# Performance work log

Measured on AMD Instinct MI355X. Metric: run time of the kernel, lower is better.

## Reference

```python
import jax, jax.numpy as jnp
import numpy as np

H = 768
NH = 12
HD = H // NH
FF = 3072
EPS = 1e-12
SCALE = 1.0 / (HD ** 0.5)


def _ln(x, g, b):
    m = jnp.mean(x, axis=-1, keepdims=True)
    v = jnp.mean((x - m) ** 2, axis=-1, keepdims=True)
    return (x - m) * jax.lax.rsqrt(v + EPS) * g + b


def setup_inputs() -> dict:
    key = jax.random.key(0)
    ks = jax.random.split(key, 16)
    B, Q, S, T = 8, 64, 48, 128
    s = 0.02
    return {
        "q": jax.random.normal(ks[0], (B, Q, H), jnp.float32),
        "k": jax.random.normal(ks[1], (B, S, T, H), jnp.float32),
        "mask": jax.random.randint(ks[2], (B, S, T), 0, 2, jnp.int32),
        "Wq": jax.random.normal(ks[3], (H, H), jnp.float32) * s,
        "Wkv": jax.random.normal(ks[4], (H, H), jnp.float32) * s,
        "Wo": jax.random.normal(ks[5], (H, H), jnp.float32) * s,
        "bo": jnp.zeros((H,), jnp.float32),
        "ln1_g": jnp.ones((H,), jnp.float32),
        "ln1_b": jnp.zeros((H,), jnp.float32),
        "W1": jax.random.normal(ks[6], (H, FF), jnp.float32) * s,
        "b1": jnp.zeros((FF,), jnp.float32),
        "W2": jax.random.normal(ks[7], (FF, H), jnp.float32) * s,
        "b2": jnp.zeros((H,), jnp.float32),
        "ln2_g": jnp.ones((H,), jnp.float32),
        "ln2_b": jnp.zeros((H,), jnp.float32),
    }


def reference(q, k, mask, Wq, Wkv, Wo, bo, ln1_g, ln1_b, W1, b1, W2, b2, ln2_g, ln2_b):
    B, Q, _ = q.shape
    _, S, T, _ = k.shape
    # projections (no bias)
    qp = (q @ Wq).reshape(B, Q, NH, HD)            # [b,q,h,d]
    kv = (k @ Wkv).reshape(B, S, T, NH, HD)        # [b,s,t,h,d]
    # broadcast-query grouped attention: softmax only over token dim t
    scores = jnp.einsum('bqhd,bsthd->bhqst', qp, kv) * SCALE
    scores = scores + mask.astype(scores.dtype)[:, None, None, :, :] * -10000.0
    alpha = jax.nn.softmax(scores, axis=-1)        # dropout is identity in eval
    res = jnp.einsum('bhqst,bsthd->bqshd', alpha, kv).reshape(B, Q, S, H)
    # BertSelfOutput with zero residual (residual=False)
    attn_out = _ln(res @ Wo + bo, ln1_g, ln1_b)    # [b,q,s,H]
    # FFN
    ffn = jax.nn.gelu(attn_out @ W1 + b1, approximate=False) @ W2 + b2
    return _ln(attn_out + ffn, ln2_g, ln2_b)
```

## Files before the change

### kernel.cpp

```cpp
#include <hip/hip_runtime.h>
#include <hip/hip_bf16.h>
#include <math.h>

#define B_ 8
#define Q_ 64
#define S_ 48
#define T_ 128
#define H_ 768
#define NH_ 12
#define HD_ 64
#define FF_ 3072

typedef float f32x4 __attribute__((ext_vector_type(4)));
typedef short s16x8 __attribute__((ext_vector_type(8)));
typedef short s16x4 __attribute__((ext_vector_type(4)));

__device__ __forceinline__ float ldT(const float* p, size_t i) { return p[i]; }
__device__ __forceinline__ float ldT(const __hip_bfloat16* p, size_t i) { return __bfloat162float(p[i]); }
__device__ __forceinline__ void stT(float* p, size_t i, float v) { p[i] = v; }
__device__ __forceinline__ void stT(__hip_bfloat16* p, size_t i, float v) { p[i] = __float2bfloat16(v); }

__device__ __forceinline__ short f2bf(float f) {
  __hip_bfloat16 h = __float2bfloat16(f);
  return *reinterpret_cast<short*>(&h);
}

__device__ __forceinline__ float gelu_f(float x) {
  return 0.5f * x * (1.0f + erff(x * 0.70710678118654752f));
}

__device__ __forceinline__ void gld_lds16(const void* g, void* l) {
  __builtin_amdgcn_global_load_lds(
      (const __attribute__((address_space(1))) void*)g,
      (__attribute__((address_space(3))) void*)l, 16, 0, 0);
}

#define FENCE() asm volatile("" ::: "memory")
#define BARRIER() do { FENCE(); __builtin_amdgcn_s_barrier(); FENCE(); } while (0)
#define WAITV(n) asm volatile("s_waitcnt vmcnt(" #n ")" ::: "memory")

template<int K, typename OT, bool BIAS, bool GELU>
__global__ __launch_bounds__(512, 2) void gemm8p(
    const __hip_bfloat16* __restrict__ A,
    const __hip_bfloat16* __restrict__ BT,
    const float* __restrict__ bias, OT* __restrict__ C,
    int N, int nbx)
{
  constexpr int NT = K / 64;
  static_assert(NT % 3 == 0, "K/64 must be divisible by 3");
  __shared__ __align__(16) char sm[3 * 49152];

  int wg = blockIdx.x;
  const int q8 = gridDim.x >> 3;
  wg = (wg & 7) * q8 + (wg >> 3);
  const int bm = wg / nbx;
  const int bn = wg % nbx;
  const int m0 = bm * 128, n0 = bn * 256;

  const int tid = threadIdx.x;
  const int lane = tid & 63;
  const int wid = tid >> 6;
  const int wr = wid >> 2;
  const int wc = wid & 3;
  const int kcg = lane >> 4;
  const int rl = lane & 15;

  const __hip_bfloat16* gA[2];
  const __hip_bfloat16* gB[4];
  #pragma unroll
  for (int r = 0; r < 2; ++r) {
    const int c = tid + r * 512, row = c >> 3, slot = c & 7;
    const int kc = slot ^ (row & 7);
    gA[r] = A + (size_t)(m0 + row) * K + kc * 8;
  }
  #pragma unroll
  for (int r = 0; r < 4; ++r) {
    const int c = tid + r * 512, row = c >> 3, slot = c & 7;
    const int kc = slot ^ (row & 7);
    gB[r] = BT + (size_t)(n0 + row) * K + kc * 8;
  }

  auto stageA = [&](char* bb) {
    gld_lds16(gA[0], bb + tid * 16);
    gld_lds16(gA[1], bb + (tid + 512) * 16);
    gA[0] += 64; gA[1] += 64;
  };
  auto stageB1 = [&](char* bb) {
    gld_lds16(gB[0], bb + 16384 + tid * 16);
    gld_lds16(gB[1], bb + 16384 + (tid + 512) * 16);
    gB[0] += 64; gB[1] += 64;
  };
  auto stageB2 = [&](char* bb) {
    gld_lds16(gB[2], bb + 16384 + (tid + 1024) * 16);
    gld_lds16(gB[3], bb + 16384 + (tid + 1536) * 16);
    gB[2] += 64; gB[3] += 64;
  };

  int offA[4][2], offB[4][2];
  #pragma unroll
  for (int mf = 0; mf < 4; ++mf)
    #pragma unroll
    for (int kch = 0; kch < 2; ++kch) {
      const int row = wr * 64 + mf * 16 + rl;
      const int ch = kch * 4 + kcg;
      offA[mf][kch] = row * 128 + ((ch ^ (row & 7)) << 4);
    }
  #pragma unroll
  for (int nf = 0; nf < 4; ++nf)
    #pragma unroll
    for (int kch = 0; kch < 2; ++kch) {
      const int row = wc * 64 + nf * 16 + rl;
      const int ch = kch * 4 + kcg;
      offB[nf][kch] = 16384 + row * 128 + ((ch ^ (row & 7)) << 4);
    }

  f32x4 acc[4][4] = {};

  stageA(sm); stageB1(sm); stageB2(sm);
  stageA(sm + 49152); stageB1(sm + 49152); stageB2(sm + 49152);
  WAITV(6);
  BARRIER();

  auto tile_body = [&](char* cb, char* nb, bool doStage, bool last) {
    s16x8 af[4][2], bf[4][2];
    #pragma unroll
    for (int mf = 0; mf < 2; ++mf)
      #pragma unroll
      for (int kch = 0; kch < 2; ++kch)
        af[mf][kch] = *(const s16x8*)(cb + offA[mf][kch]);
    #pragma unroll
    for (int nf = 0; nf < 2; ++nf)
      #pragma unroll
      for (int kch = 0; kch < 2; ++kch)
        bf[nf][kch] = *(const s16x8*)(cb + offB[nf][kch]);
    if (doStage) stageA(nb);
    BARRIER();
    __builtin_amdgcn_s_setprio(1);
    #pragma unroll
    for (int kch = 0; kch < 2; ++kch)
      #pragma unroll
      for (int mf = 0; mf < 2; ++mf)
        #pragma unroll
        for (int nf = 0; nf < 2; ++nf)
          acc[mf][nf] = __builtin_amdgcn_mfma_f32_16x16x32_bf16(
              af[mf][kch], bf[nf][kch], acc[mf][nf], 0, 0, 0);
    __builtin_amdgcn_s_setprio(0);
    BARRIER();
    #pragma unroll
    for (int nf = 2; nf < 4; ++nf)
      #pragma unroll
      for (int kch = 0; kch < 2; ++kch)
        bf[nf][kch] = *(const s16x8*)(cb + offB[nf][kch]);
    if (doStage) stageB1(nb);
    BARRIER();
    __builtin_amdgcn_s_setprio(1);
    #pragma unroll
    for (int kch = 0; kch < 2; ++kch)
      #pragma unroll
      for (int mf = 0; mf < 2; ++mf)
        #pragma unroll
        for (int nf = 2; nf < 4; ++nf)
          acc[mf][nf] = __builtin_amdgcn_mfma_f32_16x16x32_bf16(
              af[mf][kch], bf[nf][kch], acc[mf][nf], 0, 0, 0);
    __builtin_amdgcn_s_setprio(0);
    BARRIER();
    #pragma unroll
    for (int mf = 2; mf < 4; ++mf)
      #pragma unroll
      for (int kch = 0; kch < 2; ++kch)
        af[mf][kch] = *(const s16x8*)(cb + offA[mf][kch]);
    if (doStage) stageB2(nb);
    BARRIER();
    __builtin_amdgcn_s_setprio(1);
    #pragma unroll
    for (int kch = 0; kch < 2; ++kch)
      #pragma unroll
      for (int mf = 2; mf < 4; ++mf)
        #pragma unroll
        for (int nf = 0; nf < 2; ++nf)
          acc[mf][nf] = __builtin_amdgcn_mfma_f32_16x16x32_bf16(
              af[mf][kch], bf[nf][kch], acc[mf][nf], 0, 0, 0);
    __builtin_amdgcn_s_setprio(0);
    BARRIER();
    __builtin_amdgcn_s_setprio(1);
    #pragma unroll
    for (int kch = 0; kch < 2; ++kch)
      #pragma unroll
      for (int mf = 2; mf < 4; ++mf)
        #pragma unroll
        for (int nf = 2; nf < 4; ++nf)
          acc[mf][nf] = __builtin_amdgcn_mfma_f32_16x16x32_bf16(
              af[mf][kch], bf[nf][kch], acc[mf][nf], 0, 0, 0);
    __builtin_amdgcn_s_setprio(0);
    if (!last) {
      if (doStage) WAITV(6);
      else         WAITV(0);
      BARRIER();
    }
  };

  char* b0 = sm;
  char* b1 = sm + 49152;
  char* b2 = sm + 2 * 49152;
  #pragma unroll 1
  for (int t = 0; t < NT; t += 3) {
    tile_body(b0, b2, t + 2 < NT, t + 1 == NT);
    tile_body(b1, b0, t + 3 < NT, t + 2 == NT);
    tile_body(b2, b1, t + 4 < NT, t + 3 == NT);
  }

  const int colb = n0 + wc * 64 + rl;
  const int rowb = m0 + wr * 64 + (lane >> 4) * 4;
  float bv[4];
  #pragma unroll
  for (int nf = 0; nf < 4; ++nf) bv[nf] = BIAS ? bias[colb + nf * 16] : 0.0f;
  #pragma unroll
  for (int mf = 0; mf < 4; ++mf) {
    #pragma unroll
    for (int r = 0; r < 4; ++r) {
      const int row = rowb + mf * 16 + r;
      #pragma unroll
      for (int nf = 0; nf < 4; ++nf) {
        float v = acc[mf][nf][r] + bv[nf];
        if (GELU) v = gelu_f(v);
        stT(C, (size_t)row * N + colb + nf * 16, v);
      }
    }
  }
}

template<typename OT>
__global__ __launch_bounds__(256) void gemm64(
    const float* __restrict__ A, const float* __restrict__ W,
    OT* __restrict__ C, int M, int N, int K)
{
  __shared__ float As[16][65];
  __shared__ float Ws[16][65];
  const int tid = threadIdx.x;
  const int m0 = blockIdx.y * 64;
  const int n0 = blockIdx.x * 64;
  const int tx = (tid & 15) * 4;
  const int ty = (tid >> 4) * 4;
  float acc[4][4] = {};

  for (int k0 = 0; k0 < K; k0 += 16) {
    #pragma unroll
    for (int r = 0; r < 4; ++r) {
      int idx = tid + r * 256;
      int mm = idx >> 4, kk = idx & 15;
      As[kk][mm] = A[(size_t)(m0 + mm) * K + (k0 + kk)];
    }
    #pragma unroll
    for (int r = 0; r < 4; ++r) {
      int idx = tid + r * 256;
      int kk = idx >> 6, nn = idx & 63;
      Ws[kk][nn] = W[(size_t)(k0 + kk) * N + (n0 + nn)];
    }
    __syncthreads();
    #pragma unroll
    for (int kk = 0; kk < 16; ++kk) {
      float a[4], b[4];
      #pragma unroll
      for (int i = 0; i < 4; ++i) a[i] = As[kk][ty + i];
      #pragma unroll
      for (int j = 0; j < 4; ++j) b[j] = Ws[kk][tx + j];
      #pragma unroll
      for (int i = 0; i < 4; ++i)
        #pragma unroll
        for (int j = 0; j < 4; ++j) acc[i][j] += a[i] * b[j];
    }
    __syncthreads();
  }
  #pragma unroll
  for (int i = 0; i < 4; ++i)
    #pragma unroll
    for (int j = 0; j < 4; ++j)
      stT(C, (size_t)(m0 + ty + i) * N + (n0 + tx + j), acc[i][j]);
}

__global__ __launch_bounds__(256) void transpose_cast(
    const float* __restrict__ W, __hip_bfloat16* __restrict__ WT, int K, int N)
{
  __shared__ float t[32][33];
  const int n0 = blockIdx.x * 32, k0 = blockIdx.y * 32;
  const int x = threadIdx.x & 31, y4 = (threadIdx.x >> 5) * 4;
  #pragma unroll
  for (int i = 0; i < 4; ++i)
    t[y4 + i][x] = W[(size_t)(k0 + y4 + i) * N + n0 + x];
  __syncthreads();
  #pragma unroll
  for (int i = 0; i < 4; ++i)
    WT[(size_t)(n0 + y4 + i) * K + k0 + x] = __float2bfloat16(t[x][y4 + i]);
}

__global__ __launch_bounds__(256) void cast_f32_bf16(
    const float* __restrict__ x, __hip_bfloat16* __restrict__ y, size_t n4)
{
  const size_t i = (size_t)blockIdx.x * 256 + threadIdx.x;
  if (i >= n4) return;
  const float4 v = ((const float4*)x)[i];
  __hip_bfloat16 o[4] = { __float2bfloat16(v.x), __float2bfloat16(v.y),
                          __float2bfloat16(v.z), __float2bfloat16(v.w) };
  *(ushort4*)(y + i * 4) = *(ushort4*)o;
}

__global__ __launch_bounds__(256) void attn_mfma(
    const __hip_bfloat16* __restrict__ qp,
    const __hip_bfloat16* __restrict__ kvp,
    const int* __restrict__ mask,
    __hip_bfloat16* __restrict__ res)
{
  const int s = blockIdx.x, h = blockIdx.y, b = blockIdx.z;
  __shared__ __align__(16) char lds[66048];
  char* Ks = lds;
  char* VT = lds + 16384;
  char* SC = lds + 32768;
  float* mv = (float*)(lds + 65536);

  const int tid = threadIdx.x;
  const int lane = tid & 63;
  const int wid = tid >> 6;
  const int wr = wid >> 1, wc = wid & 1;
  const int kcg = lane >> 4, rl = lane & 15;

  if (tid < 128) mv[tid] = (float)mask[((size_t)b * S_ + s) * T_ + tid] * -10000.0f;

  {
    const __hip_bfloat16* qb = qp + ((size_t)b * Q_) * H_ + h * HD_;
    #pragma unroll
    for (int r = 0; r < 2; ++r) {
      const int c = tid + r * 256;
      const int qq = c >> 3, sc = c & 7;
      const int kc8 = sc ^ (qq & 7);
      gld_lds16(qb + (size_t)qq * H_ + kc8 * 8, SC + c * 16);
    }
  }
  {
    const int kc8 = tid & 7, tg = tid >> 3;
    const int t0 = tg * 4;
    const __hip_bfloat16* kb = kvp + (((size_t)b * S_ + s) * T_) * H_ + h * HD_ + kc8 * 8;
    s16x8 r0 = *(const s16x8*)(kb + (size_t)(t0 + 0) * H_);
    s16x8 r1 = *(const s16x8*)(kb + (size_t)(t0 + 1) * H_);
    s16x8 r2 = *(const s16x8*)(kb + (size_t)(t0 + 2) * H_);
    s16x8 r3 = *(const s16x8*)(kb + (size_t)(t0 + 3) * H_);
    *(s16x8*)(Ks + (t0 + 0) * 128 + ((kc8 ^ ((t0 + 0) & 7)) << 4)) = r0;
    *(s16x8*)(Ks + (t0 + 1) * 128 + ((kc8 ^ ((t0 + 1) & 7)) << 4)) = r1;
    *(s16x8*)(Ks + (t0 + 2) * 128 + ((kc8 ^ ((t0 + 2) & 7)) << 4)) = r2;
    *(s16x8*)(Ks + (t0 + 3) * 128 + ((kc8 ^ ((t0 + 3) & 7)) << 4)) = r3;
    const int tc = tg >> 1;
    const int toff = (tg & 1) * 8;
    #pragma unroll
    for (int j = 0; j < 8; ++j) {
      s16x4 v4 = { r0[j], r1[j], r2[j], r3[j] };
      const int d = kc8 * 8 + j;
      *(s16x4*)(VT + d * 256 + ((tc ^ (d & 15)) << 4) + toff) = v4;
    }
  }
  __syncthreads();

  f32x4 acc[2][4] = {};
  {
    s16x8 af[2][2], bf[2][4];
    #pragma unroll
    for (int kk = 0; kk < 2; ++kk) {
      #pragma unroll
      for (int m = 0; m < 2; ++m) {
        const int q = wr * 32 + m * 16 + rl;
        const int kc8 = kk * 4 + kcg;
        af[kk][m] = *(const s16x8*)(SC + q * 128 + ((kc8 ^ (q & 7)) << 4));
      }
      #pragma unroll
      for (int n = 0; n < 4; ++n) {
        const int t = wc * 64 + n * 16 + rl;
        const int kc8 = kk * 4 + kcg;
        bf[kk][n] = *(const s16x8*)(Ks + t * 128 + ((kc8 ^ (t & 7)) << 4));
      }
    }
    #pragma unroll
    for (int kk = 0; kk < 2; ++kk)
      #pragma unroll
      for (int m = 0; m < 2; ++m)
        #pragma unroll
        for (int n = 0; n < 4; ++n)
          acc[m][n] = __builtin_amdgcn_mfma_f32_16x16x32_bf16(af[kk][m], bf[kk][n], acc[m][n], 0, 0, 0);
  }
  __syncthreads();

  #pragma unroll
  for (int m = 0; m < 2; ++m)
    #pragma unroll
    for (int n = 0; n < 4; ++n)
      #pragma unroll
      for (int r = 0; r < 4; ++r) {
        const int q = wr * 32 + m * 16 + (lane >> 4) * 4 + r;
        const int t = wc * 64 + n * 16 + rl;
        const int tc32 = t >> 2;
        *(float*)(SC + q * 512 + ((tc32 ^ (q & 31)) << 4) + (t & 3) * 4) =
            acc[m][n][r] * 0.125f + mv[t];
      }
  __syncthreads();

  {
    const int q = tid >> 2, quarter = tid & 3;
    float vals[32];
    #pragma unroll
    for (int j = 0; j < 8; ++j) {
      const int tc32 = quarter * 8 + j;
      const f32x4 c = *(const f32x4*)(SC + q * 512 + ((tc32 ^ (q & 31)) << 4));
      vals[j * 4 + 0] = c[0]; vals[j * 4 + 1] = c[1];
      vals[j * 4 + 2] = c[2]; vals[j * 4 + 3] = c[3];
    }
    float mx = -1e30f;
    #pragma unroll
    for (int i = 0; i < 32; ++i) mx = fmaxf(mx, vals[i]);
    mx = fmaxf(mx, __shfl_xor(mx, 1, 64));
    mx = fmaxf(mx, __shfl_xor(mx, 2, 64));
    float sum = 0.0f;
    #pragma unroll
    for (int i = 0; i < 32; ++i) { vals[i] = expf(vals[i] - mx); sum += vals[i]; }
    sum += __shfl_xor(sum, 1, 64);
    sum += __shfl_xor(sum, 2, 64);
    const float inv = 1.0f / sum;
    #pragma unroll
    for (int jj = 0; jj < 4; ++jj) {
      const int tcp = quarter * 4 + jj;
      s16x8 pk;
      #pragma unroll
      for (int i = 0; i < 8; ++i) pk[i] = f2bf(vals[jj * 8 + i] * inv);
      *(s16x8*)(SC + q * 512 + ((tcp ^ (q & 15)) << 4)) = pk;
    }
  }
  __syncthreads();

  f32x4 oacc[2][2] = {};
  #pragma unroll
  for (int kt = 0; kt < 4; ++kt) {
    s16x8 pa[2], vb[2];
    #pragma unroll
    for (int m = 0; m < 2; ++m) {
      const int q = wr * 32 + m * 16 + rl;
      const int tcp = kt * 4 + kcg;
      pa[m] = *(const s16x8*)(SC + q * 512 + ((tcp ^ (q & 15)) << 4));
    }
    #pragma unroll
    for (int n = 0; n < 2; ++n) {
      const int d = wc * 32 + n * 16 + rl;
      const int tc = kt * 4 + kcg;
      vb[n] = *(const s16x8*)(VT + d * 256 + ((tc ^ (d & 15)) << 4));
    }
    #pragma unroll
    for (int m = 0; m < 2; ++m)
      #pragma unroll
      for (int n = 0; n < 2; ++n)
        oacc[m][n] = __builtin_amdgcn_mfma_f32_16x16x32_bf16(pa[m], vb[n], oacc[m][n], 0, 0, 0);
  }
  #pragma unroll
  for (int m = 0; m < 2; ++m)
    #pragma unroll
    for (int n = 0; n < 2; ++n)
      #pragma unroll
      for (int r = 0; r < 4; ++r) {
        const int q = wr * 32 + m * 16 + (lane >> 4) * 4 + r;
        const int d = wc * 32 + n * 16 + rl;
        res[(((size_t)b * Q_ + q) * S_ + s) * H_ + h * HD_ + d] =
            __float2bfloat16(oacc[m][n][r]);
      }
}

template<bool ADD, typename IT, typename OT>
__global__ __launch_bounds__(256) void ln_kernel(
    const IT* __restrict__ X, const IT* __restrict__ X2,
    const float* __restrict__ g, const float* __restrict__ bta,
    OT* __restrict__ Y)
{
  const size_t row = blockIdx.x;
  const int tid = threadIdx.x;
  float v[3];
  #pragma unroll
  for (int i = 0; i < 3; ++i) {
    int c = tid + i * 256;
    v[i] = ldT(X, row * H_ + c);
    if (ADD) v[i] += ldT(X2, row * H_ + c);
  }
  float sum = v[0] + v[1] + v[2];
  #pragma unroll
  for (int off = 32; off > 0; off >>= 1) sum += __shfl_down(sum, off, 64);
  __shared__ float red[8];
  const int w = tid >> 6;
  if ((tid & 63) == 0) red[w] = sum;
  __syncthreads();
  const float mean = (red[0] + red[1] + red[2] + red[3]) * (1.0f / 768.0f);
  float vs = 0.0f;
  #pragma unroll
  for (int i = 0; i < 3; ++i) { v[i] -= mean; vs += v[i] * v[i]; }
  #pragma unroll
  for (int off = 32; off > 0; off >>= 1) vs += __shfl_down(vs, off, 64);
  if ((tid & 63) == 0) red[4 + w] = vs;
  __syncthreads();
  const float rstd = rsqrtf((red[4] + red[5] + red[6] + red[7]) * (1.0f / 768.0f) + 1e-12f);
  #pragma unroll
  for (int i = 0; i < 3; ++i) {
    int c = tid + i * 256;
    stT(Y, row * H_ + c, v[i] * rstd * g[c] + bta[c]);
  }
}

extern "C" void kernel_launch(void* const* d_in, const int* in_sizes, int n_in,
                              void* d_out, int out_size, void* d_ws, size_t ws_size,
                              hipStream_t stream) {
  const float* q    = (const float*)d_in[0];
  const float* k    = (const float*)d_in[1];
  const int*   mask = (const int*)d_in[2];
  const float* Wq   = (const float*)d_in[3];
  const float* Wkv  = (const float*)d_in[4];
  const float* Wo   = (const float*)d_in[5];
  const float* bo   = (const float*)d_in[6];
  const float* ln1g = (const float*)d_in[7];
  const float* ln1b = (const float*)d_in[8];
  const float* W1   = (const float*)d_in[9];
  const float* b1   = (const float*)d_in[10];
  const float* W2   = (const float*)d_in[11];
  const float* b2   = (const float*)d_in[12];
  const float* ln2g = (const float*)d_in[13];
  const float* ln2b = (const float*)d_in[14];
  float* out = (float*)d_out;

  const int MROWS = B_ * Q_ * S_;
  const int KVROWS = B_ * S_ * T_;

  char* ws = (char*)d_ws;
  __hip_bfloat16* kbf  = (__hip_bfloat16*)ws;
  __hip_bfloat16* kvp  = (__hip_bfloat16*)(ws + 75497472);
  __hip_bfloat16* ffn1 = (__hip_bfloat16*)ws;
  __hip_bfloat16* ares = (__hip_bfloat16*)(ws + 150994944);
  __hip_bfloat16* ffn2 = ares;
  __hip_bfloat16* aln  = (__hip_bfloat16*)(ws + 188743680);
  __hip_bfloat16* qp   = (__hip_bfloat16*)(ws + 226492416);
  __hip_bfloat16* WkvT = (__hip_bfloat16*)(ws + 228065280);
  __hip_bfloat16* WoT  = (__hip_bfloat16*)(ws + 229244928);
  __hip_bfloat16* W1T  = (__hip_bfloat16*)(ws + 230424576);
  __hip_bfloat16* W2T  = (__hip_bfloat16*)(ws + 235143168);

  dim3 blk(256);
  dim3 blk8(512);

  transpose_cast<<<dim3(24, 24), blk, 0, stream>>>(Wkv, WkvT, H_, H_);
  transpose_cast<<<dim3(24, 24), blk, 0, stream>>>(Wo, WoT, H_, H_);
  transpose_cast<<<dim3(96, 24), blk, 0, stream>>>(W1, W1T, H_, FF_);
  transpose_cast<<<dim3(24, 96), blk, 0, stream>>>(W2, W2T, FF_, H_);
  cast_f32_bf16<<<dim3((KVROWS * H_ / 4 + 255) / 256), blk, 0, stream>>>(
      k, kbf, (size_t)KVROWS * H_ / 4);

  gemm64<__hip_bfloat16><<<dim3(H_ / 64, 512 / 64), blk, 0, stream>>>(
      q, Wq, qp, 512, H_, H_);
  gemm8p<768, __hip_bfloat16, false, false>
      <<<dim3((KVROWS / 128) * (H_ / 256)), blk8, 0, stream>>>(
      kbf, WkvT, nullptr, kvp, H_, H_ / 256);
  attn_mfma<<<dim3(S_, NH_, B_), blk, 0, stream>>>(qp, kvp, mask, ares);
  gemm8p<768, float, true, false>
      <<<dim3((MROWS / 128) * (H_ / 256)), blk8, 0, stream>>>(
      ares, WoT, bo, out, H_, H_ / 256);
  ln_kernel<false, float, __hip_bfloat16><<<MROWS, blk, 0, stream>>>(
      out, nullptr, ln1g, ln1b, aln);
  gemm8p<768, __hip_bfloat16, true, true>
      <<<dim3((MROWS / 128) * (FF_ / 256)), blk8, 0, stream>>>(
      aln, W1T, b1, ffn1, FF_, FF_ / 256);
  gemm8p<3072, __hip_bfloat16, true, false>
      <<<dim3((MROWS / 128) * (H_ / 256)), blk8, 0, stream>>>(
      ffn1, W2T, b2, ffn2, H_, H_ / 256);
  ln_kernel<true, __hip_bfloat16, float><<<MROWS, blk, 0, stream>>>(
      aln, ffn2, ln2g, ln2b, out);
}
```

Baseline: 679.7 us.

## Enlarge GEMM tiles to 256x256 with a nine-slot LDS ring pipeline

```diff
diff --git a/kernel.cpp b/kernel.cpp
--- a/kernel.cpp
+++ b/kernel.cpp
@@ -40,182 +40,162 @@
 #define WAITV(n) asm volatile("s_waitcnt vmcnt(" #n ")" ::: "memory")
 
 template<int K, typename OT, bool BIAS, bool GELU>
-__global__ __launch_bounds__(512, 2) void gemm8p(
+__global__ __launch_bounds__(512, 2) void gemm9r(
     const __hip_bfloat16* __restrict__ A,
     const __hip_bfloat16* __restrict__ BT,
     const float* __restrict__ bias, OT* __restrict__ C,
     int N, int nbx)
 {
   constexpr int NT = K / 64;
-  static_assert(NT % 3 == 0, "K/64 must be divisible by 3");
-  __shared__ __align__(16) char sm[3 * 49152];
+  static_assert(NT >= 3, "need at least 3 K-tiles");
+  __shared__ __align__(16) char sm[9 * 16384];
 
   int wg = blockIdx.x;
   const int q8 = gridDim.x >> 3;
   wg = (wg & 7) * q8 + (wg >> 3);
   const int bm = wg / nbx;
   const int bn = wg % nbx;
-  const int m0 = bm * 128, n0 = bn * 256;
+  const int m0 = bm * 256, n0 = bn * 256;
 
   const int tid = threadIdx.x;
   const int lane = tid & 63;
   const int wid = tid >> 6;
-  const int wr = wid >> 2;
+  const int wm = wid >> 2;
   const int wc = wid & 3;
+  const int bh = wc >> 1;
   const int kcg = lane >> 4;
   const int rl = lane & 15;
 
-  const __hip_bfloat16* gA[2];
-  const __hip_bfloat16* gB[4];
-  #pragma unroll
-  for (int r = 0; r < 2; ++r) {
-    const int c = tid + r * 512, row = c >> 3, slot = c & 7;
-    const int kc = slot ^ (row & 7);
-    gA[r] = A + (size_t)(m0 + row) * K + kc * 8;
-  }
-  #pragma unroll
-  for (int r = 0; r < 4; ++r) {
-    const int c = tid + r * 512, row = c >> 3, slot = c & 7;
-    const int kc = slot ^ (row & 7);
-    gB[r] = BT + (size_t)(n0 + row) * K + kc * 8;
-  }
-
-  auto stageA = [&](char* bb) {
-    gld_lds16(gA[0], bb + tid * 16);
-    gld_lds16(gA[1], bb + (tid + 512) * 16);
-    gA[0] += 64; gA[1] += 64;
+  const int c1r = tid >> 3;
+  const int c1k = (tid & 7) ^ (c1r & 7);
+
+  auto stage_slot = [&](int slot) {
+    const int tile = slot >> 2, half = slot & 3;
+    const __hip_bfloat16* mb =
+        (half < 2 ? A + (size_t)m0 * K : BT + (size_t)n0 * K)
+        + (size_t)(half & 1) * 128 * K + tile * 64;
+    char* lb = sm + (slot % 9) * 16384;
+    gld_lds16(mb + (size_t)c1r * K + c1k * 8, lb + tid * 16);
+    gld_lds16(mb + (size_t)(c1r + 64) * K + c1k * 8, lb + (tid + 512) * 16);
   };
-  auto stageB1 = [&](char* bb) {
-    gld_lds16(gB[0], bb + 16384 + tid * 16);
-    gld_lds16(gB[1], bb + 16384 + (tid + 512) * 16);
-    gB[0] += 64; gB[1] += 64;
-  };
-  auto stageB2 = [&](char* bb) {
-    gld_lds16(gB[2], bb + 16384 + (tid + 1024) * 16);
-    gld_lds16(gB[3], bb + 16384 + (tid + 1536) * 16);
-    gB[2] += 64; gB[3] += 64;
-  };
-
-  int offA[4][2], offB[4][2];
-  #pragma unroll
-  for (int mf = 0; mf < 4; ++mf)
-    #pragma unroll
-    for (int kch = 0; kch < 2; ++kch) {
-      const int row = wr * 64 + mf * 16 + rl;
-      const int ch = kch * 4 + kcg;
-      offA[mf][kch] = row * 128 + ((ch ^ (row & 7)) << 4);
-    }
-  #pragma unroll
-  for (int nf = 0; nf < 4; ++nf)
-    #pragma unroll
-    for (int kch = 0; kch < 2; ++kch) {
-      const int row = wc * 64 + nf * 16 + rl;
-      const int ch = kch * 4 + kcg;
-      offB[nf][kch] = 16384 + row * 128 + ((ch ^ (row & 7)) << 4);
-    }
-
-  f32x4 acc[4][4] = {};
-
-  stageA(sm); stageB1(sm); stageB2(sm);
-  stageA(sm + 49152); stageB1(sm + 49152); stageB2(sm + 49152);
-  WAITV(6);
+
+  int woffA[8], woffB[4];
+  #pragma unroll
+  for (int mf = 0; mf < 8; ++mf) {
+    const int lr = mf * 16 + rl;
+    woffA[mf] = lr * 128 + ((kcg ^ (lr & 7)) << 4);
+  }
+  #pragma unroll
+  for (int nf = 0; nf < 4; ++nf) {
+    const int lr = (wc & 1) * 64 + nf * 16 + rl;
+    woffB[nf] = lr * 128 + ((kcg ^ (lr & 7)) << 4);
+  }
+
+  f32x4 acc[8][4] = {};
+
+  stage_slot(0); stage_slot(1); stage_slot(2); stage_slot(3); stage_slot(4);
+  WAITV(2);
   BARRIER();
 
-  auto tile_body = [&](char* cb, char* nb, bool doStage, bool last) {
-    s16x8 af[4][2], bf[4][2];
-    #pragma unroll
-    for (int mf = 0; mf < 2; ++mf)
+  int ringT = 0;
+  #pragma unroll 1
+  for (int t = 0; t < NT; ++t) {
+    int rA = ringT + wm;      if (rA >= 9) rA -= 9;
+    int rB = ringT + 2 + bh;  if (rB >= 9) rB -= 9;
+    const char* baseA = sm + rA * 16384;
+    const char* baseB = sm + rB * 16384;
+
+    s16x8 af0[4][2], af1[4][2], bf[2][2];
+
+    #pragma unroll
+    for (int mf = 0; mf < 4; ++mf)
       #pragma unroll
       for (int kch = 0; kch < 2; ++kch)
-        af[mf][kch] = *(const s16x8*)(cb + offA[mf][kch]);
+        af0[mf][kch] = *(const s16x8*)(baseA + (woffA[mf] ^ (kch << 6)));
     #pragma unroll
     for (int nf = 0; nf < 2; ++nf)
       #pragma unroll
       for (int kch = 0; kch < 2; ++kch)
-        bf[nf][kch] = *(const s16x8*)(cb + offB[nf][kch]);
-    if (doStage) stageA(nb);
+        bf[nf][kch] = *(const s16x8*)(baseB + (woffB[nf] ^ (kch << 6)));
+    if (4 * t + 5 < 4 * NT) stage_slot(4 * t + 5);
     BARRIER();
     __builtin_amdgcn_s_setprio(1);
     #pragma unroll
     for (int kch = 0; kch < 2; ++kch)
       #pragma unroll
-      for (int mf = 0; mf < 2; ++mf)
+      for (int mf = 0; mf < 4; ++mf)
         #pragma unroll
         for (int nf = 0; nf < 2; ++nf)
           acc[mf][nf] = __builtin_amdgcn_mfma_f32_16x16x32_bf16(
-              af[mf][kch], bf[nf][kch], acc[mf][nf], 0, 0, 0);
+              af0[mf][kch], bf[nf][kch], acc[mf][nf], 0, 0, 0);
     __builtin_amdgcn_s_setprio(0);
     BARRIER();
-    #pragma unroll
-    for (int nf = 2; nf < 4; ++nf)
+
+    #pragma unroll
+    for (int mf = 0; mf < 4; ++mf)
       #pragma unroll
       for (int kch = 0; kch < 2; ++kch)
-        bf[nf][kch] = *(const s16x8*)(cb + offB[nf][kch]);
-    if (doStage) stageB1(nb);
+        af1[mf][kch] = *(const s16x8*)(baseA + (woffA[4 + mf] ^ (kch << 6)));
+    if (4 * t + 6 < 4 * NT) stage_slot(4 * t + 6);
     BARRIER();
     __builtin_amdgcn_s_setprio(1);
     #pragma unroll
     for (int kch = 0; kch < 2; ++kch)
       #pragma unroll
-      for (int mf = 0; mf < 2; ++mf)
+      for (int mf = 0; mf < 4; ++mf)
         #pragma unroll
-        for (int nf = 2; nf < 4; ++nf)
-          acc[mf][nf] = __builtin_amdgcn_mfma_f32_16x16x32_bf16(
-              af[mf][kch], bf[nf][kch], acc[mf][nf], 0, 0, 0);
+        for (int nf = 0; nf < 2; ++nf)
+          acc[4 + mf][nf] = __builtin_amdgcn_mfma_f32_16x16x32_bf16(
+              af1[mf][kch], bf[nf][kch], acc[4 + mf][nf], 0, 0, 0);
     __builtin_amdgcn_s_setprio(0);
     BARRIER();
-    #pragma unroll
-    for (int mf = 2; mf < 4; ++mf)
+
+    #pragma unroll
+    for (int nf = 0; nf < 2; ++nf)
       #pragma unroll
       for (int kch = 0; kch < 2; ++kch)
-        af[mf][kch] = *(const s16x8*)(cb + offA[mf][kch]);
-    if (doStage) stageB2(nb);
+        bf[nf][kch] = *(const s16x8*)(baseB + (woffB[2 + nf] ^ (kch << 6)));
+    if (4 * t + 7 < 4 * NT) stage_slot(4 * t + 7);
     BARRIER();
     __builtin_amdgcn_s_setprio(1);
     #pragma unroll
     for (int kch = 0; kch < 2; ++kch)
       #pragma unroll
-      for (int mf = 2; mf < 4; ++mf)
+      for (int mf = 0; mf < 4; ++mf)
         #pragma unroll
         for (int nf = 0; nf < 2; ++nf)
-          acc[mf][nf] = __builtin_amdgcn_mfma_f32_16x16x32_bf16(
-              af[mf][kch], bf[nf][kch], acc[mf][nf], 0, 0, 0);
+          acc[4 + mf][2 + nf] = __builtin_amdgcn_mfma_f32_16x16x32_bf16(
+              af1[mf][kch], bf[nf][kch], acc[4 + mf][2 + nf], 0, 0, 0);
     __builtin_amdgcn_s_setprio(0);
     BARRIER();
+
+    if (4 * t + 8 < 4 * NT) stage_slot(4 * t + 8);
     __builtin_amdgcn_s_setprio(1);
     #pragma unroll
     for (int kch = 0; kch < 2; ++kch)
       #pragma unroll
-      for (int mf = 2; mf < 4; ++mf)
+      for (int mf = 0; mf < 4; ++mf)
         #pragma unroll
-        for (int nf = 2; nf < 4; ++nf)
-          acc[mf][nf] = __builtin_amdgcn_mfma_f32_16x16x32_bf16(
-              af[mf][kch], bf[nf][kch], acc[mf][nf], 0, 0, 0);
+        for (int nf = 0; nf < 2; ++nf)
+          acc[mf][2 + nf] = __builtin_amdgcn_mfma_f32_16x16x32_bf16(
+              af0[mf][kch], bf[nf][kch], acc[mf][2 + nf], 0, 0, 0);
     __builtin_amdgcn_s_setprio(0);
-    if (!last) {
-      if (doStage) WAITV(6);
-      else         WAITV(0);
+
+    if (t < NT - 1) {
+      if (t < NT - 2) WAITV(2);
+      else            WAITV(0);
       BARRIER();
     }
-  };
-
-  char* b0 = sm;
-  char* b1 = sm + 49152;
-  char* b2 = sm + 2 * 49152;
-  #pragma unroll 1
-  for (int t = 0; t < NT; t += 3) {
-    tile_body(b0, b2, t + 2 < NT, t + 1 == NT);
-    tile_body(b1, b0, t + 3 < NT, t + 2 == NT);
-    tile_body(b2, b1, t + 4 < NT, t + 3 == NT);
+    ringT += 4; if (ringT >= 9) ringT -= 9;
   }
 
   const int colb = n0 + wc * 64 + rl;
-  const int rowb = m0 + wr * 64 + (lane >> 4) * 4;
+  const int rowb = m0 + wm * 128 + (lane >> 4) * 4;
   float bv[4];
   #pragma unroll
   for (int nf = 0; nf < 4; ++nf) bv[nf] = BIAS ? bias[colb + nf * 16] : 0.0f;
   #pragma unroll
-  for (int mf = 0; mf < 4; ++mf) {
+  for (int mf = 0; mf < 8; ++mf) {
     #pragma unroll
     for (int r = 0; r < 4; ++r) {
       const int row = rowb + mf * 16 + r;
@@ -542,7 +522,7 @@
   __hip_bfloat16* W2T  = (__hip_bfloat16*)(ws + 235143168);
 
   dim3 blk(256);
-  dim3 blk8(512);
+  dim3 blk9(512);
 
   transpose_cast<<<dim3(24, 24), blk, 0, stream>>>(Wkv, WkvT, H_, H_);
   transpose_cast<<<dim3(24, 24), blk, 0, stream>>>(Wo, WoT, H_, H_);
@@ -553,20 +533,20 @@
 
   gemm64<__hip_bfloat16><<<dim3(H_ / 64, 512 / 64), blk, 0, stream>>>(
       q, Wq, qp, 512, H_, H_);
-  gemm8p<768, __hip_bfloat16, false, false>
-      <<<dim3((KVROWS / 128) * (H_ / 256)), blk8, 0, stream>>>(
+  gemm9r<768, __hip_bfloat16, false, false>
+      <<<dim3((KVROWS / 256) * (H_ / 256)), blk9, 0, stream>>>(
       kbf, WkvT, nullptr, kvp, H_, H_ / 256);
   attn_mfma<<<dim3(S_, NH_, B_), blk, 0, stream>>>(qp, kvp, mask, ares);
-  gemm8p<768, float, true, false>
-      <<<dim3((MROWS / 128) * (H_ / 256)), blk8, 0, stream>>>(
+  gemm9r<768, float, true, false>
+      <<<dim3((MROWS / 256) * (H_ / 256)), blk9, 0, stream>>>(
       ares, WoT, bo, out, H_, H_ / 256);
   ln_kernel<false, float, __hip_bfloat16><<<MROWS, blk, 0, stream>>>(
       out, nullptr, ln1g, ln1b, aln);
-  gemm8p<768, __hip_bfloat16, true, true>
-      <<<dim3((MROWS / 128) * (FF_ / 256)), blk8, 0, stream>>>(
+  gemm9r<768, __hip_bfloat16, true, true>
+      <<<dim3((MROWS / 256) * (FF_ / 256)), blk9, 0, stream>>>(
       aln, W1T, b1, ffn1, FF_, FF_ / 256);
-  gemm8p<3072, __hip_bfloat16, true, false>
-      <<<dim3((MROWS / 128) * (H_ / 256)), blk8, 0, stream>>>(
+  gemm9r<3072, __hip_bfloat16, true, false>
+      <<<dim3((MROWS / 256) * (H_ / 256)), blk9, 0, stream>>>(
       ffn1, W2T, b2, ffn2, H_, H_ / 256);
   ln_kernel<true, __hip_bfloat16, float><<<MROWS, blk, 0, stream>>>(
       aln, ffn2, ln2g, ln2b, out);
```

Measured after the change: 797.6 us. 1.17x slower.
